# Kernel tuning notes

Measured on AMD Instinct MI355X. Metric: run time of the kernel, lower is better.

## Reference

```python
import math
import jax, jax.numpy as jnp
import numpy as np

OLEN = 512
RATIO = 0.5
DROP_P = 0.2


def _gat(x, src, dst, W, a_s, a_d, b):
    """PyG GATConv (heads=1, concat=True, add_self_loops=True, neg_slope=0.2)."""
    n = x.shape[0]
    loops = jnp.arange(n, dtype=src.dtype)
    s = jnp.concatenate([src, loops])  # [E+N] source nodes
    d = jnp.concatenate([dst, loops])  # [E+N] destination nodes
    h = x @ W                           # [N, H]
    alpha_s = h @ a_s                   # [N]
    alpha_d = h @ a_d                   # [N]
    e = jax.nn.leaky_relu(alpha_s[s] + alpha_d[d], 0.2)  # [E+N]
    # segment softmax over destination neighborhoods
    m = jax.ops.segment_max(e, d, num_segments=n)
    ee = jnp.exp(e - m[d])
    denom = jax.ops.segment_sum(ee, d, num_segments=n)
    alpha = ee / denom[d]
    out = jax.ops.segment_sum(alpha[:, None] * h[s], d, num_segments=n)
    return out + b


def _forward(x, src, dst, W1, a_src1, a_dst1, b1, W2, a_src2, a_dst2, b2,
             W3, a_src3, a_dst3, b3, W_rel, W_root, b_pool):
    N, E = x.shape[0], src.shape[0]
    key = jax.random.key(42)
    h = x
    for i, (W, a_s, a_d, b) in enumerate([(W1, a_src1, a_dst1, b1),
                                          (W2, a_src2, a_dst2, b2),
                                          (W3, a_src3, a_dst3, b3)]):
        h = jax.nn.relu(_gat(h, src, dst, W, a_s, a_d, b))
        keep = jax.random.bernoulli(jax.random.fold_in(key, i), 1.0 - DROP_P, h.shape)
        h = jnp.where(keep, h / (1.0 - DROP_P), 0.0)  # F.dropout(training=True)

    # SAGPooling(GraphConv score, ratio=0.5, tanh) repeated until n <= 512.
    # Node counts are static per iteration (k = ceil(0.5*n)); edge arrays keep
    # fixed size E with a validity mask (edges dropped when an endpoint is pooled away).
    cur_src, cur_dst = src, dst
    emask = jnp.ones((E,), dtype=h.dtype)
    n = N
    while True:
        agg = jax.ops.segment_sum(h[cur_src] * emask[:, None], cur_dst, num_segments=n)
        score = (agg @ W_rel + h @ W_root + b_pool)[:, 0]  # GraphConv(d->1), aggr='add'
        score = jnp.tanh(score)
        k = math.ceil(RATIO * n)
        top_vals, perm = jax.lax.top_k(score, k)
        h = h[perm] * top_vals[:, None]
        inv = jnp.full((n,), -1, dtype=cur_src.dtype).at[perm].set(
            jnp.arange(k, dtype=cur_src.dtype))
        ns, nd = inv[cur_src], inv[cur_dst]
        valid = (ns >= 0) & (nd >= 0)
        emask = emask * valid.astype(emask.dtype)
        cur_src = jnp.where(valid, ns, 0)
        cur_dst = jnp.where(valid, nd, 0)
        n = k
        if n <= OLEN:
            break

    out = jnp.zeros((OLEN, h.shape[1]), h.dtype).at[:n].set(h)
    return out


def setup_inputs() -> dict:
    key = jax.random.key(0)
    ks = jax.random.split(key, 20)
    N, E, IDIM, HDIM = 50000, 800000, 128, 200
    inp = {
        "x": jax.random.normal(ks[0], (N, IDIM), jnp.float32),
        "src": jax.random.randint(ks[1], (E,), 0, N, jnp.int32),
        "dst": jax.random.randint(ks[2], (E,), 0, N, jnp.int32),
    }
    def w(k, shape, fan_in):
        return jax.random.normal(k, shape, jnp.float32) / np.sqrt(fan_in).astype(np.float32)
    inp["W1"] = w(ks[3], (IDIM, HDIM), IDIM)
    inp["a_src1"] = w(ks[4], (HDIM,), HDIM)
    inp["a_dst1"] = w(ks[5], (HDIM,), HDIM)
    inp["b1"] = jnp.zeros((HDIM,), jnp.float32)
    inp["W2"] = w(ks[6], (HDIM, HDIM), HDIM)
    inp["a_src2"] = w(ks[7], (HDIM,), HDIM)
    inp["a_dst2"] = w(ks[8], (HDIM,), HDIM)
    inp["b2"] = jnp.zeros((HDIM,), jnp.float32)
    inp["W3"] = w(ks[9], (HDIM, HDIM), HDIM)
    inp["a_src3"] = w(ks[10], (HDIM,), HDIM)
    inp["a_dst3"] = w(ks[11], (HDIM,), HDIM)
    inp["b3"] = jnp.zeros((HDIM,), jnp.float32)
    inp["W_rel"] = w(ks[12], (HDIM, 1), HDIM)
    inp["W_root"] = w(ks[13], (HDIM, 1), HDIM)
    inp["b_pool"] = jnp.zeros((1,), jnp.float32)
    return inp


def reference(x, src, dst, W1, a_src1, a_dst1, b1, W2, a_src2, a_dst2, b2,
              W3, a_src3, a_dst3, b3, W_rel, W_root, b_pool):
    return _forward(x, src, dst, W1, a_src1, a_dst1, b1, W2, a_src2, a_dst2, b2,
                    W3, a_src3, a_dst3, b3, W_rel, W_root, b_pool)
```

## Files before the change

### kernel.cpp

```cpp
#include <hip/hip_runtime.h>
#include <cstdint>
#include <cstddef>


__host__ __device__ inline void tf_round(uint32_t &x0, uint32_t &x1, int r) {
  x0 += x1;
  x1 = (x1 << r) | (x1 >> (32 - r));
  x1 ^= x0;
}

__host__ __device__ inline void threefry2x32(uint32_t k0, uint32_t k1,
                                             uint32_t &x0, uint32_t &x1) {
  uint32_t ks2 = k0 ^ k1 ^ 0x1BD11BDAu;
  x0 += k0; x1 += k1;
  tf_round(x0, x1, 13); tf_round(x0, x1, 15); tf_round(x0, x1, 26); tf_round(x0, x1, 6);
  x0 += k1; x1 += ks2 + 1u;
  tf_round(x0, x1, 17); tf_round(x0, x1, 29); tf_round(x0, x1, 16); tf_round(x0, x1, 24);
  x0 += ks2; x1 += k0 + 2u;
  tf_round(x0, x1, 13); tf_round(x0, x1, 15); tf_round(x0, x1, 26); tf_round(x0, x1, 6);
  x0 += k0; x1 += k1 + 3u;
  tf_round(x0, x1, 17); tf_round(x0, x1, 29); tf_round(x0, x1, 16); tf_round(x0, x1, 24);
  x0 += k1; x1 += ks2 + 4u;
  tf_round(x0, x1, 13); tf_round(x0, x1, 15); tf_round(x0, x1, 26); tf_round(x0, x1, 6);
  x0 += ks2; x1 += k0 + 5u;
}

__global__ __launch_bounds__(256) void gemm200_k(
    const float* __restrict__ A, const float* __restrict__ B,
    float* __restrict__ C, int M, int K) {
  __shared__ float As[128 * 9];
  __shared__ __align__(16) float Bs[8][208];
  int tid = threadIdx.x;
  int m0 = blockIdx.x * 128;
  int r = tid >> 2;
  int colBase = (tid & 3) * 52;
  int nq = (colBase == 156) ? 11 : 13;
  float acc0[52], acc1[52];
#pragma unroll
  for (int q = 0; q < 52; q++) { acc0[q] = 0.f; acc1[q] = 0.f; }

  int arow = tid >> 1;
  int ac = (tid & 1) * 4;
  int gmA = m0 + arow;
  const float* Aptr = A + (size_t)gmA * K + ac;
  int bk0 = tid / 50, bc0 = (tid - bk0 * 50) * 4;
  int t2 = tid + 256;
  int bk1 = t2 / 50, bc1 = (t2 - bk1 * 50) * 4;
  bool hasB1 = (t2 < 400);

  float4 va = make_float4(0.f, 0.f, 0.f, 0.f);
  if (gmA < M) va = *(const float4*)(Aptr);
  float4 vb0 = *(const float4*)(B + (size_t)bk0 * 200 + bc0);
  float4 vb1 = make_float4(0.f, 0.f, 0.f, 0.f);
  if (hasB1) vb1 = *(const float4*)(B + (size_t)bk1 * 200 + bc1);

  for (int k0 = 0; k0 < K; k0 += 8) {
    As[arow * 9 + ac + 0] = va.x;
    As[arow * 9 + ac + 1] = va.y;
    As[arow * 9 + ac + 2] = va.z;
    As[arow * 9 + ac + 3] = va.w;
    *(float4*)(&Bs[bk0][bc0]) = vb0;
    if (hasB1) *(float4*)(&Bs[bk1][bc1]) = vb1;
    __syncthreads();
    int kn = k0 + 8;
    if (kn < K) {
      if (gmA < M) va = *(const float4*)(Aptr + kn);
      vb0 = *(const float4*)(B + (size_t)(kn + bk0) * 200 + bc0);
      if (hasB1) vb1 = *(const float4*)(B + (size_t)(kn + bk1) * 200 + bc1);
    }
#pragma unroll
    for (int kk = 0; kk < 8; kk++) {
      float a0 = As[r * 9 + kk];
      float a1 = As[(r + 64) * 9 + kk];
#pragma unroll
      for (int q = 0; q < 13; q++) {
        float4 b = *(const float4*)(&Bs[kk][colBase + 4 * q]);
        acc0[4 * q + 0] += a0 * b.x; acc0[4 * q + 1] += a0 * b.y;
        acc0[4 * q + 2] += a0 * b.z; acc0[4 * q + 3] += a0 * b.w;
        acc1[4 * q + 0] += a1 * b.x; acc1[4 * q + 1] += a1 * b.y;
        acc1[4 * q + 2] += a1 * b.z; acc1[4 * q + 3] += a1 * b.w;
      }
    }
    __syncthreads();
  }
  int gm0 = m0 + r, gm1 = m0 + r + 64;
#pragma unroll
  for (int q = 0; q < 13; q++) {
    if (q < nq) {
      int col = colBase + 4 * q;
      float4 v0 = make_float4(acc0[4 * q + 0], acc0[4 * q + 1],
                              acc0[4 * q + 2], acc0[4 * q + 3]);
      float4 v1 = make_float4(acc1[4 * q + 0], acc1[4 * q + 1],
                              acc1[4 * q + 2], acc1[4 * q + 3]);
      if (gm0 < M) *(float4*)(C + (size_t)gm0 * 200 + col) = v0;
      if (gm1 < M) *(float4*)(C + (size_t)gm1 * 200 + col) = v1;
    }
  }
}

__global__ __launch_bounds__(256) void dual_dot_k(
    const float* __restrict__ H, const float* __restrict__ v1,
    const float* __restrict__ v2, float* __restrict__ o1,
    float* __restrict__ o2, int n) {
  int wave = blockIdx.x * 4 + (threadIdx.x >> 6);
  int lane = threadIdx.x & 63;
  if (wave >= n) return;
  const float* row = H + (size_t)wave * 200;
  float s1 = 0.f, s2 = 0.f;
  for (int d = lane; d < 200; d += 64) {
    float h = row[d];
    s1 += h * v1[d];
    s2 += h * v2[d];
  }
  for (int off = 32; off; off >>= 1) {
    s1 += __shfl_down(s1, off);
    s2 += __shfl_down(s2, off);
  }
  if (lane == 0) { o1[wave] = s1; o2[wave] = s2; }
}

__global__ __launch_bounds__(256) void indeg_k(const int* __restrict__ dst,
                                               int* __restrict__ cnt, int E) {
  int e = blockIdx.x * 256 + threadIdx.x;
  if (e < E) atomicAdd(&cnt[dst[e]], 1);
}

__global__ __launch_bounds__(256) void scan_k(const int* __restrict__ cnt,
                                              int* __restrict__ rowptr, int N) {
  __shared__ int psum[256];
  int t = threadIdx.x;
  int CH = (N + 255) / 256;
  int beg = t * CH, end = min(beg + CH, N);
  if (beg > N) { beg = N; }
  int s = 0;
  for (int i = beg; i < end; i++) s += cnt[i];
  psum[t] = s;
  __syncthreads();
  if (t == 0) {
    int run = 0;
    for (int i = 0; i < 256; i++) { int v = psum[i]; psum[i] = run; run += v; }
  }
  __syncthreads();
  int run = psum[t];
  for (int i = beg; i < end; i++) { rowptr[i] = run; run += cnt[i]; }
  if (end == N && beg <= N) rowptr[N] = run;
}

__global__ __launch_bounds__(256) void cpyint_k(const int* __restrict__ a,
                                                int* __restrict__ b, int n) {
  int i = blockIdx.x * 256 + threadIdx.x;
  if (i < n) b[i] = a[i];
}

__global__ __launch_bounds__(256) void place_k(const int* __restrict__ dst,
                                               int* __restrict__ curs,
                                               int* __restrict__ csr, int E) {
  int e = blockIdx.x * 256 + threadIdx.x;
  if (e >= E) return;
  int pos = atomicAdd(&curs[dst[e]], 1);
  csr[pos] = e;
}

__global__ __launch_bounds__(256) void sortrow_k(const int* __restrict__ rowptr,
                                                 int* __restrict__ csr, int N) {
  int d = blockIdx.x * 256 + threadIdx.x;
  if (d >= N) return;
  int b = rowptr[d], e2 = rowptr[d + 1];
  for (int i = b + 1; i < e2; i++) {
    int v = csr[i];
    int j = i - 1;
    while (j >= b && csr[j] > v) { csr[j + 1] = csr[j]; j--; }
    csr[j + 1] = v;
  }
}

__device__ inline float dec_ord(unsigned enc) {
  unsigned b = (enc & 0x80000000u) ? (enc ^ 0x80000000u) : ~enc;
  return __uint_as_float(b);
}

__device__ inline unsigned enc_ord(float ev) {
  unsigned b = __float_as_uint(ev);
  return (b & 0x80000000u) ? ~b : (b | 0x80000000u);
}

__global__ __launch_bounds__(256) void eeden_k(
    const int* __restrict__ rowptr, const int* __restrict__ csr,
    const int* __restrict__ src, const float* __restrict__ as_,
    const float* __restrict__ ad_, int2* __restrict__ pk,
    float* __restrict__ eeS, float* __restrict__ den, int N) {
  int d = blockIdx.x * 256 + threadIdx.x;
  if (d >= N) return;
  float adv = ad_[d];
  int b = rowptr[d], e2 = rowptr[d + 1];
  unsigned mx = 0u;
  for (int i = b; i < e2; i++) {
    int sv = src[csr[i]];
    float v = as_[sv] + adv;
    float ev = (v >= 0.f) ? v : 0.2f * v;
    mx = max(mx, enc_ord(ev));
  }
  {
    float v = as_[d] + adv;
    float ev = (v >= 0.f) ? v : 0.2f * v;
    mx = max(mx, enc_ord(ev));
  }
  float m = dec_ord(mx);
  float s = 0.f;
  for (int i = b; i < e2; i++) {
    int sv = src[csr[i]];
    float v = as_[sv] + adv;
    float ev = (v >= 0.f) ? v : 0.2f * v;
    float ee = expf(ev - m);
    pk[i] = make_int2(sv, __float_as_int(ee));
    s = __fadd_rn(s, ee);
  }
  float vS = as_[d] + adv;
  float evS = (vS >= 0.f) ? vS : 0.2f * vS;
  float eS = expf(evS - m);
  eeS[d] = eS;
  s = __fadd_rn(s, eS);
  den[d] = s;
}

#define GLD(s) (*(const float4*)(Hl + (size_t)(s) * 200))
#define ACC(W_, H_)                                    \
  acc.x = __fadd_rn(acc.x, __fmul_rn((W_), (H_).x));   \
  acc.y = __fadd_rn(acc.y, __fmul_rn((W_), (H_).y));   \
  acc.z = __fadd_rn(acc.z, __fmul_rn((W_), (H_).z));   \
  acc.w = __fadd_rn(acc.w, __fmul_rn((W_), (H_).w));

__global__ __launch_bounds__(256) void gat_out_k(
    const int* __restrict__ rowptr, const int2* __restrict__ pk,
    const float* __restrict__ eeS, const float* __restrict__ den,
    const float* __restrict__ HW, const float* __restrict__ bias,
    float* __restrict__ OUT, uint32_t tk0, uint32_t tk1, int N) {
  int node = blockIdx.x * 4 + (threadIdx.x >> 6);
  int lane = threadIdx.x & 63;
  if (node >= N || lane >= 50) return;
  int b = rowptr[node];
  int deg = rowptr[node + 1] - b;
  int cnt = deg + 1;
  float dn = den[node];
  const float* __restrict__ Hl = HW + 4 * lane;

  auto fS = [&](int t, int &s, float &w) {
    if (t < deg) {
      int2 p = pk[b + t];
      s = p.x;
      w = __fdiv_rn(__int_as_float(p.y), dn);
    } else if (t == deg) {
      s = node;
      w = __fdiv_rn(eeS[node], dn);
    } else {
      s = node;
      w = 0.f;
    }
  };

  int sa, sb, sc, sd, se, sf, sn;
  float w0, w1, w2, w3, w4, w5, wn;
  fS(0, sa, w0); fS(1, sb, w1); fS(2, sc, w2); fS(3, sd, w3);
  float4 h0 = GLD(sa), h1 = GLD(sb), h2 = GLD(sc), h3 = GLD(sd);
  fS(4, se, w4);
  fS(5, sf, w5);

  float4 acc = make_float4(0.f, 0.f, 0.f, 0.f);
  for (int t = 0; t < cnt; t++) {
    float4 h4 = GLD(se);
    fS(t + 6, sn, wn);
    ACC(w0, h0);
    h0 = h1; h1 = h2; h2 = h3; h3 = h4;
    w0 = w1; w1 = w2; w2 = w3; w3 = w4; w4 = w5; w5 = wn;
    se = sf; sf = sn;
  }

  float4 bv4 = *(const float4*)(bias + 4 * lane);
  float vin[4] = {acc.x, acc.y, acc.z, acc.w};
  float bb4[4] = {bv4.x, bv4.y, bv4.z, bv4.w};
  float vout[4];
  int tbase = node * 200 + 4 * lane;
#pragma unroll
  for (int j = 0; j < 4; j++) {
    uint32_t x0 = 0u, x1 = (uint32_t)(tbase + j);
    threefry2x32(tk0, tk1, x0, x1);
    uint32_t bits = x0 ^ x1;
    float u = __uint_as_float((bits >> 9) | 0x3f800000u) - 1.0f;
    float v = vin[j] + bb4[j];
    v = fmaxf(v, 0.f);
    vout[j] = (u < 0.8f) ? (v / 0.8f) : 0.f;
  }
  *(float4*)(OUT + (size_t)node * 200 + 4 * lane) =
      make_float4(vout[0], vout[1], vout[2], vout[3]);
}

__global__ __launch_bounds__(256) void einit_k(
    const int* __restrict__ src, const int* __restrict__ dst,
    int* __restrict__ cs, int* __restrict__ cd, int* __restrict__ orig,
    int E, int N) {
  int e = blockIdx.x * 256 + threadIdx.x;
  if (e < E) { cs[e] = src[e]; cd[e] = dst[e]; }
  if (e < N) orig[e] = e;
}

__global__ __launch_bounds__(256) void pool_agg_k(
    const int* __restrict__ rowptr, const int* __restrict__ csr,
    const int* __restrict__ csrc, const int* __restrict__ orig,
    const float* __restrict__ H, const float* __restrict__ wrel,
    const float* __restrict__ wroot, const float* __restrict__ bp,
    float* __restrict__ score, int n) {
  __shared__ float sagg[4][200];
  int wv = threadIdx.x >> 6;
  int node = blockIdx.x * 4 + wv;
  int lane = threadIdx.x & 63;
  if (node >= n) return;
  int o = orig[node];
  int b = rowptr[o];
  int deg = rowptr[o + 1] - b;

  if (lane < 50) {
    const float* __restrict__ Hl = H + 4 * lane;
    auto fS = [&](int t, int &s, float &w) {
      if (t < deg) {
        int e = csr[b + t];
        int sv = csrc[e];
        s = (sv >= 0) ? sv : 0;
        w = (sv >= 0) ? 1.f : 0.f;
      } else {
        s = 0;
        w = 0.f;
      }
    };

    int sa, sb, sc, sd, se, sf, sn;
    float w0, w1, w2, w3, w4, w5, wn;
    fS(0, sa, w0); fS(1, sb, w1); fS(2, sc, w2); fS(3, sd, w3);
    float4 h0 = GLD(sa), h1 = GLD(sb), h2 = GLD(sc), h3 = GLD(sd);
    fS(4, se, w4);
    fS(5, sf, w5);

    float4 acc = make_float4(0.f, 0.f, 0.f, 0.f);
    for (int t = 0; t < deg; t++) {
      float4 h4 = GLD(se);
      fS(t + 6, sn, wn);
      ACC(w0, h0);
      h0 = h1; h1 = h2; h2 = h3; h3 = h4;
      w0 = w1; w1 = w2; w2 = w3; w3 = w4; w4 = w5; w5 = wn;
      se = sf; sf = sn;
    }
    sagg[wv][4 * lane + 0] = acc.x;
    sagg[wv][4 * lane + 1] = acc.y;
    sagg[wv][4 * lane + 2] = acc.z;
    sagg[wv][4 * lane + 3] = acc.w;
  }
  __threadfence_block();

  const float* arow = sagg[wv];
  const float* hrow = H + (size_t)node * 200;
  float s1 = 0.f, s2 = 0.f;
  for (int d = lane; d < 200; d += 64) {
    s1 += arow[d] * wrel[d];
    s2 += hrow[d] * wroot[d];
  }
  for (int off = 32; off; off >>= 1) {
    s1 += __shfl_down(s1, off);
    s2 += __shfl_down(s2, off);
  }
  if (lane == 0) score[node] = tanhf((s1 + s2) + bp[0]);
}
#undef GLD
#undef ACC


__global__ __launch_bounds__(256) void rhenc_k(const float* __restrict__ score,
                                               unsigned* __restrict__ keyA,
                                               int* __restrict__ payA,
                                               int* __restrict__ counts,
                                               int n, int NB) {
  __shared__ int hist[256];
  hist[threadIdx.x] = 0;
  __syncthreads();
  int i = blockIdx.x * 256 + threadIdx.x;
  if (i < n) {
    unsigned b = __float_as_uint(score[i]);
    if (b == 0x80000000u) b = 0u;
    unsigned key = ~enc_ord(__uint_as_float(b));
    keyA[i] = key;
    payA[i] = i;
    atomicAdd(&hist[key & 255u], 1);
  }
  __syncthreads();
  counts[threadIdx.x * NB + blockIdx.x] = hist[threadIdx.x];
}

__global__ __launch_bounds__(256) void rscan_k(int* __restrict__ counts,
                                               int* __restrict__ base, int NB) {
  __shared__ int tot[256];
  int t = threadIdx.x;
  int s = 0;
  for (int b = 0; b < NB; b++) s += counts[t * NB + b];
  tot[t] = s;
  __syncthreads();
  if (t == 0) {
    int run = 0;
    for (int i = 0; i < 256; i++) { int v = tot[i]; tot[i] = run; run += v; }
  }
  __syncthreads();
  int run = tot[t];
  for (int b = 0; b < NB; b++) {
    int c = counts[t * NB + b];
    base[t * NB + b] = run;
    run += c;
    counts[t * NB + b] = 0;
  }
}

__global__ __launch_bounds__(256) void rscatter_k(
    const unsigned* __restrict__ keyIn, const int* __restrict__ payIn,
    const int* __restrict__ base, unsigned* __restrict__ keyOut,
    int* __restrict__ payOut, int* __restrict__ countsNext,
    int n, int NB, int shift) {
  __shared__ int dig[256];
  int t = threadIdx.x;
  int i = blockIdx.x * 256 + t;
  unsigned k = 0u;
  int p = 0, d = -1;
  if (i < n) {
    k = keyIn[i];
    p = payIn[i];
    d = (int)((k >> shift) & 255u);
  }
  dig[t] = d;
  __syncthreads();
  if (i < n) {
    int local = 0;
    for (int j = 0; j < t; j++) local += (dig[j] == d) ? 1 : 0;
    int pos = base[d * NB + blockIdx.x] + local;
    keyOut[pos] = k;
    payOut[pos] = p;
    int nd = (int)((k >> (shift + 8)) & 255u);
    atomicAdd(&countsNext[nd * NB + (pos >> 8)], 1);
  }
}

__global__ __launch_bounds__(256) void rscatterF_k(
    const unsigned* __restrict__ keyIn, const int* __restrict__ payIn,
    const int* __restrict__ base, const int* __restrict__ oin,
    int* __restrict__ oout, int* __restrict__ perm, int* __restrict__ inv,
    int n, int NB, int k) {
  __shared__ int dig[256];
  int t = threadIdx.x;
  int i = blockIdx.x * 256 + t;
  int p = 0, d = -1;
  if (i < n) {
    p = payIn[i];
    d = (int)((keyIn[i] >> 24) & 255u);
  }
  dig[t] = d;
  __syncthreads();
  if (i < n) {
    int local = 0;
    for (int j = 0; j < t; j++) local += (dig[j] == d) ? 1 : 0;
    int pos = base[d * NB + blockIdx.x] + local;
    if (pos < k) { perm[pos] = p; inv[p] = pos; oout[pos] = oin[p]; }
    else inv[p] = -1;
  }
}

__global__ __launch_bounds__(256) void gather_k(
    const float* __restrict__ H, const int* __restrict__ perm,
    const float* __restrict__ score, float* __restrict__ Ho, int k) {
  int r = blockIdx.x;
  int d = threadIdx.x;
  int p = perm[r];
  float s = score[p];
  if (d < 200) Ho[(size_t)r * 200 + d] = __fmul_rn(H[(size_t)p * 200 + d], s);
}

__global__ __launch_bounds__(256) void remap_k(int* __restrict__ cs,
                                               int* __restrict__ cd,
                                               const int* __restrict__ inv, int E) {
  int e = blockIdx.x * 256 + threadIdx.x;
  if (e >= E) return;
  int a = cs[e];
  if (a < 0) return;
  int na = inv[a], nb = inv[cd[e]];
  bool valid = (na >= 0) && (nb >= 0);
  cs[e] = valid ? na : -1;
  cd[e] = valid ? nb : -1;
}

__global__ __launch_bounds__(256) void out_copy_k(const float* __restrict__ h,
                                                  float* __restrict__ out, int cnt) {
  int t = blockIdx.x * 256 + threadIdx.x;
  if (t < cnt) out[t] = h[t];
}

extern "C" void kernel_launch(void* const* d_in, const int* in_sizes, int n_in,
                              void* d_out, int out_size, void* d_ws, size_t ws_size,
                              hipStream_t stream) {
  const int ID = 128, HD = 200;
  const int N = in_sizes[0] / ID;
  const int E = in_sizes[1];

  const float* x = (const float*)d_in[0];
  const int* src = (const int*)d_in[1];
  const int* dst = (const int*)d_in[2];
  const float* W[3]   = {(const float*)d_in[3], (const float*)d_in[7], (const float*)d_in[11]};
  const float* asv[3] = {(const float*)d_in[4], (const float*)d_in[8], (const float*)d_in[12]};
  const float* adv[3] = {(const float*)d_in[5], (const float*)d_in[9], (const float*)d_in[13]};
  const float* bv[3]  = {(const float*)d_in[6], (const float*)d_in[10], (const float*)d_in[14]};
  const float* Wrel  = (const float*)d_in[15];
  const float* Wroot = (const float*)d_in[16];
  const float* bpool = (const float*)d_in[17];

  char* ws = (char*)d_ws;
  float*    bufA  = (float*)(ws + 0);
  float*    bufB  = (float*)(ws + 40000000);
  float*    as_   = (float*)(ws + 80000000);
  float*    ad_   = (float*)(ws + 80200000);
  float*    den   = (float*)(ws + 84000000);
  float*    score = (float*)(ws + 84200000);
  int*      rank_ = (int*)(ws + 84400000);
  int*      perm_ = (int*)(ws + 84600000);
  int*      inv_  = (int*)(ws + 84800000);
  int*      origA = (int*)(ws + 85000000);
  int*      origB = (int*)(ws + 85200000);
  int*      rowptr= (int*)(ws + 85400000);
  int*      curs  = (int*)(ws + 85650000);
  int*      csr   = (int*)(ws + 85850000);
  int*      csrc  = (int*)(ws + 89050000);
  int*      cdst  = (int*)(ws + 92250000);

  int2* pk = (int2*)(ws + 89050000);
  float* eeS = (float*)(ws + 80400000);

  char* rx = ws + 80400000;
  unsigned* keyA   = (unsigned*)(rx + 0 * 262144);
  unsigned* keyB   = (unsigned*)(rx + 1 * 262144);
  int*      payA   = (int*)(rx + 2 * 262144);
  int*      payB   = (int*)(rx + 3 * 262144);
  int*      rcounts= (int*)(rx + 4 * 262144);
  int*      rbase  = (int*)(rx + 5 * 262144);

  uint32_t fk0[3], fk1[3];
  for (int i = 0; i < 3; i++) {
    uint32_t a = 0u, b = (uint32_t)i;
    threefry2x32(0u, 42u, a, b);
    fk0[i] = a; fk1[i] = b;
  }

  const int B256 = 256;
  hipMemsetAsync(rank_, 0, (size_t)N * 4, stream);
  indeg_k<<<(E + 255) / 256, B256, 0, stream>>>(dst, rank_, E);
  scan_k<<<1, B256, 0, stream>>>(rank_, rowptr, N);
  cpyint_k<<<(N + 255) / 256, B256, 0, stream>>>(rowptr, curs, N);
  place_k<<<(E + 255) / 256, B256, 0, stream>>>(dst, curs, csr, E);
  sortrow_k<<<(N + 255) / 256, B256, 0, stream>>>(rowptr, csr, N);

  for (int i = 0; i < 3; i++) {
    const float* in = (i == 0) ? x : bufB;
    int K = (i == 0) ? ID : HD;
    gemm200_k<<<(N + 127) / 128, B256, 0, stream>>>(in, W[i], bufA, N, K);
    dual_dot_k<<<(N + 3) / 4, B256, 0, stream>>>(bufA, asv[i], adv[i], as_, ad_, N);
    eeden_k<<<(N + 255) / 256, B256, 0, stream>>>(rowptr, csr, src, as_, ad_,
                                                  pk, eeS, den, N);
    gat_out_k<<<(N + 3) / 4, B256, 0, stream>>>(rowptr, pk, eeS, den, bufA,
                                                bv[i], bufB, fk0[i], fk1[i], N);
  }

  einit_k<<<(E + 255) / 256, B256, 0, stream>>>(src, dst, csrc, cdst, origA, E, N);
  float* hcur = bufB;
  float* hnext = bufA;
  int* ocur = origA;
  int* onext = origB;
  int n = N;
  while (true) {
    int k = (n + 1) / 2;
    int NB = (n + 255) / 256;
    pool_agg_k<<<(n + 3) / 4, B256, 0, stream>>>(rowptr, csr, csrc, ocur, hcur,
                                                 Wrel, Wroot, bpool, score, n);
    rhenc_k<<<NB, B256, 0, stream>>>(score, keyA, payA, rcounts, n, NB);
    rscan_k<<<1, B256, 0, stream>>>(rcounts, rbase, NB);
    rscatter_k<<<NB, B256, 0, stream>>>(keyA, payA, rbase, keyB, payB, rcounts, n, NB, 0);
    rscan_k<<<1, B256, 0, stream>>>(rcounts, rbase, NB);
    rscatter_k<<<NB, B256, 0, stream>>>(keyB, payB, rbase, keyA, payA, rcounts, n, NB, 8);
    rscan_k<<<1, B256, 0, stream>>>(rcounts, rbase, NB);
    rscatter_k<<<NB, B256, 0, stream>>>(keyA, payA, rbase, keyB, payB, rcounts, n, NB, 16);
    rscan_k<<<1, B256, 0, stream>>>(rcounts, rbase, NB);
    rscatterF_k<<<NB, B256, 0, stream>>>(keyB, payB, rbase, ocur, onext, perm_, inv_,
                                         n, NB, k);
    gather_k<<<k, B256, 0, stream>>>(hcur, perm_, score, hnext, k);
    remap_k<<<(E + 255) / 256, B256, 0, stream>>>(csrc, cdst, inv_, E);
    { float* t = hcur; hcur = hnext; hnext = t; }
    { int* t = ocur; ocur = onext; onext = t; }
    n = k;
    if (n <= 512) break;
  }

  hipMemsetAsync(d_out, 0, (size_t)out_size * 4, stream);
  out_copy_k<<<(n * HD + 255) / 256, B256, 0, stream>>>(hcur, (float*)d_out, n * HD);
}
```

Baseline: 2.699 ms.

## Halve GEMM row tile and fuse small kernels to cut launches

```diff
diff --git a/kernel.cpp b/kernel.cpp
--- a/kernel.cpp
+++ b/kernel.cpp
@@ -28,19 +28,20 @@
 __global__ __launch_bounds__(256) void gemm200_k(
     const float* __restrict__ A, const float* __restrict__ B,
     float* __restrict__ C, int M, int K) {
-  __shared__ float As[128 * 9];
+  __shared__ float As[64 * 9];
   __shared__ __align__(16) float Bs[8][208];
   int tid = threadIdx.x;
-  int m0 = blockIdx.x * 128;
+  int m0 = blockIdx.x * 64;
   int r = tid >> 2;
   int colBase = (tid & 3) * 52;
   int nq = (colBase == 156) ? 11 : 13;
-  float acc0[52], acc1[52];
+  float acc[52];
 #pragma unroll
-  for (int q = 0; q < 52; q++) { acc0[q] = 0.f; acc1[q] = 0.f; }
+  for (int q = 0; q < 52; q++) acc[q] = 0.f;
 
   int arow = tid >> 1;
   int ac = (tid & 1) * 4;
+  bool hasA = (tid < 128);
   int gmA = m0 + arow;
   const float* Aptr = A + (size_t)gmA * K + ac;
   int bk0 = tid / 50, bc0 = (tid - bk0 * 50) * 4;
@@ -49,51 +50,47 @@
   bool hasB1 = (t2 < 400);
 
   float4 va = make_float4(0.f, 0.f, 0.f, 0.f);
-  if (gmA < M) va = *(const float4*)(Aptr);
+  if (hasA && gmA < M) va = *(const float4*)(Aptr);
   float4 vb0 = *(const float4*)(B + (size_t)bk0 * 200 + bc0);
   float4 vb1 = make_float4(0.f, 0.f, 0.f, 0.f);
   if (hasB1) vb1 = *(const float4*)(B + (size_t)bk1 * 200 + bc1);
 
   for (int k0 = 0; k0 < K; k0 += 8) {
-    As[arow * 9 + ac + 0] = va.x;
-    As[arow * 9 + ac + 1] = va.y;
-    As[arow * 9 + ac + 2] = va.z;
-    As[arow * 9 + ac + 3] = va.w;
+    if (hasA) {
+      As[arow * 9 + ac + 0] = va.x;
+      As[arow * 9 + ac + 1] = va.y;
+      As[arow * 9 + ac + 2] = va.z;
+      As[arow * 9 + ac + 3] = va.w;
+    }
     *(float4*)(&Bs[bk0][bc0]) = vb0;
     if (hasB1) *(float4*)(&Bs[bk1][bc1]) = vb1;
     __syncthreads();
     int kn = k0 + 8;
     if (kn < K) {
-      if (gmA < M) va = *(const float4*)(Aptr + kn);
+      if (hasA && gmA < M) va = *(const float4*)(Aptr + kn);
       vb0 = *(const float4*)(B + (size_t)(kn + bk0) * 200 + bc0);
       if (hasB1) vb1 = *(const float4*)(B + (size_t)(kn + bk1) * 200 + bc1);
     }
 #pragma unroll
     for (int kk = 0; kk < 8; kk++) {
       float a0 = As[r * 9 + kk];
-      float a1 = As[(r + 64) * 9 + kk];
 #pragma unroll
       for (int q = 0; q < 13; q++) {
         float4 b = *(const float4*)(&Bs[kk][colBase + 4 * q]);
-        acc0[4 * q + 0] += a0 * b.x; acc0[4 * q + 1] += a0 * b.y;
-        acc0[4 * q + 2] += a0 * b.z; acc0[4 * q + 3] += a0 * b.w;
-        acc1[4 * q + 0] += a1 * b.x; acc1[4 * q + 1] += a1 * b.y;
-        acc1[4 * q + 2] += a1 * b.z; acc1[4 * q + 3] += a1 * b.w;
+        acc[4 * q + 0] += a0 * b.x; acc[4 * q + 1] += a0 * b.y;
+        acc[4 * q + 2] += a0 * b.z; acc[4 * q + 3] += a0 * b.w;
       }
     }
     __syncthreads();
   }
-  int gm0 = m0 + r, gm1 = m0 + r + 64;
+  int gm = m0 + r;
 #pragma unroll
   for (int q = 0; q < 13; q++) {
     if (q < nq) {
       int col = colBase + 4 * q;
-      float4 v0 = make_float4(acc0[4 * q + 0], acc0[4 * q + 1],
-                              acc0[4 * q + 2], acc0[4 * q + 3]);
-      float4 v1 = make_float4(acc1[4 * q + 0], acc1[4 * q + 1],
-                              acc1[4 * q + 2], acc1[4 * q + 3]);
-      if (gm0 < M) *(float4*)(C + (size_t)gm0 * 200 + col) = v0;
-      if (gm1 < M) *(float4*)(C + (size_t)gm1 * 200 + col) = v1;
+      float4 v0 = make_float4(acc[4 * q + 0], acc[4 * q + 1],
+                              acc[4 * q + 2], acc[4 * q + 3]);
+      if (gm < M) *(float4*)(C + (size_t)gm * 200 + col) = v0;
     }
   }
 }
@@ -126,7 +123,8 @@
 }
 
 __global__ __launch_bounds__(256) void scan_k(const int* __restrict__ cnt,
-                                              int* __restrict__ rowptr, int N) {
+                                              int* __restrict__ rowptr,
+                                              int* __restrict__ curs, int N) {
   __shared__ int psum[256];
   int t = threadIdx.x;
   int CH = (N + 255) / 256;
@@ -142,14 +140,12 @@
   }
   __syncthreads();
   int run = psum[t];
-  for (int i = beg; i < end; i++) { rowptr[i] = run; run += cnt[i]; }
+  for (int i = beg; i < end; i++) {
+    rowptr[i] = run;
+    curs[i] = run;
+    run += cnt[i];
+  }
   if (end == N && beg <= N) rowptr[N] = run;
-}
-
-__global__ __launch_bounds__(256) void cpyint_k(const int* __restrict__ a,
-                                                int* __restrict__ b, int n) {
-  int i = blockIdx.x * 256 + threadIdx.x;
-  if (i < n) b[i] = a[i];
 }
 
 __global__ __launch_bounds__(256) void place_k(const int* __restrict__ dst,
@@ -317,7 +313,6 @@
   int o = orig[node];
   int b = rowptr[o];
   int deg = rowptr[o + 1] - b;
-
   if (lane < 50) {
     const float* __restrict__ Hl = H + 4 * lane;
     auto fS = [&](int t, int &s, float &w) {
@@ -331,14 +326,12 @@
         w = 0.f;
       }
     };
-
     int sa, sb, sc, sd, se, sf, sn;
     float w0, w1, w2, w3, w4, w5, wn;
     fS(0, sa, w0); fS(1, sb, w1); fS(2, sc, w2); fS(3, sd, w3);
     float4 h0 = GLD(sa), h1 = GLD(sb), h2 = GLD(sc), h3 = GLD(sd);
     fS(4, se, w4);
     fS(5, sf, w5);
-
     float4 acc = make_float4(0.f, 0.f, 0.f, 0.f);
     for (int t = 0; t < deg; t++) {
       float4 h4 = GLD(se);
@@ -354,7 +347,6 @@
     sagg[wv][4 * lane + 3] = acc.w;
   }
   __threadfence_block();
-
   const float* arow = sagg[wv];
   const float* hrow = H + (size_t)node * 200;
   float s1 = 0.f, s2 = 0.f;
@@ -370,7 +362,6 @@
 }
 #undef GLD
 #undef ACC
-
 
 __global__ __launch_bounds__(256) void rhenc_k(const float* __restrict__ score,
                                                unsigned* __restrict__ keyA,
@@ -438,8 +429,7 @@
     int pos = base[d * NB + blockIdx.x] + local;
     keyOut[pos] = k;
     payOut[pos] = p;
-    int nd = (int)((k >> (shift + 8)) & 255u);
-    atomicAdd(&countsNext[nd * NB + (pos >> 8)], 1);
+    atomicAdd(&countsNext[((k >> (shift + 8)) & 255u) * NB + (pos >> 8)], 1);
   }
 }
 
@@ -467,33 +457,37 @@
   }
 }
 
-__global__ __launch_bounds__(256) void gather_k(
+__global__ __launch_bounds__(256) void gr_k(
     const float* __restrict__ H, const int* __restrict__ perm,
-    const float* __restrict__ score, float* __restrict__ Ho, int k) {
-  int r = blockIdx.x;
-  int d = threadIdx.x;
-  int p = perm[r];
-  float s = score[p];
-  if (d < 200) Ho[(size_t)r * 200 + d] = __fmul_rn(H[(size_t)p * 200 + d], s);
-}
-
-__global__ __launch_bounds__(256) void remap_k(int* __restrict__ cs,
-                                               int* __restrict__ cd,
-                                               const int* __restrict__ inv, int E) {
-  int e = blockIdx.x * 256 + threadIdx.x;
-  if (e >= E) return;
-  int a = cs[e];
-  if (a < 0) return;
-  int na = inv[a], nb = inv[cd[e]];
-  bool valid = (na >= 0) && (nb >= 0);
-  cs[e] = valid ? na : -1;
-  cd[e] = valid ? nb : -1;
+    const float* __restrict__ score, float* __restrict__ Ho,
+    int* __restrict__ cs, int* __restrict__ cd, const int* __restrict__ inv,
+    int k, int E) {
+  int bidx = blockIdx.x;
+  if (bidx < k) {
+    int d = threadIdx.x;
+    int p = perm[bidx];
+    float s = score[p];
+    if (d < 200)
+      Ho[(size_t)bidx * 200 + d] = __fmul_rn(H[(size_t)p * 200 + d], s);
+  } else {
+    int e = (bidx - k) * 256 + threadIdx.x;
+    if (e < E) {
+      int a = cs[e];
+      if (a >= 0) {
+        int na = inv[a], nb = inv[cd[e]];
+        bool valid = (na >= 0) && (nb >= 0);
+        cs[e] = valid ? na : -1;
+        cd[e] = valid ? nb : -1;
+      }
+    }
+  }
 }
 
 __global__ __launch_bounds__(256) void out_copy_k(const float* __restrict__ h,
-                                                  float* __restrict__ out, int cnt) {
+                                                  float* __restrict__ out,
+                                                  int cnt, int total) {
   int t = blockIdx.x * 256 + threadIdx.x;
-  if (t < cnt) out[t] = h[t];
+  if (t < total) out[t] = (t < cnt) ? h[t] : 0.f;
 }
 
 extern "C" void kernel_launch(void* const* d_in, const int* in_sizes, int n_in,
@@ -553,15 +547,14 @@
   const int B256 = 256;
   hipMemsetAsync(rank_, 0, (size_t)N * 4, stream);
   indeg_k<<<(E + 255) / 256, B256, 0, stream>>>(dst, rank_, E);
-  scan_k<<<1, B256, 0, stream>>>(rank_, rowptr, N);
-  cpyint_k<<<(N + 255) / 256, B256, 0, stream>>>(rowptr, curs, N);
+  scan_k<<<1, B256, 0, stream>>>(rank_, rowptr, curs, N);
   place_k<<<(E + 255) / 256, B256, 0, stream>>>(dst, curs, csr, E);
   sortrow_k<<<(N + 255) / 256, B256, 0, stream>>>(rowptr, csr, N);
 
   for (int i = 0; i < 3; i++) {
     const float* in = (i == 0) ? x : bufB;
     int K = (i == 0) ? ID : HD;
-    gemm200_k<<<(N + 127) / 128, B256, 0, stream>>>(in, W[i], bufA, N, K);
+    gemm200_k<<<(N + 63) / 64, B256, 0, stream>>>(in, W[i], bufA, N, K);
     dual_dot_k<<<(N + 3) / 4, B256, 0, stream>>>(bufA, asv[i], adv[i], as_, ad_, N);
     eeden_k<<<(N + 255) / 256, B256, 0, stream>>>(rowptr, csr, src, as_, ad_,
                                                   pk, eeS, den, N);
@@ -590,14 +583,14 @@
     rscan_k<<<1, B256, 0, stream>>>(rcounts, rbase, NB);
     rscatterF_k<<<NB, B256, 0, stream>>>(keyB, payB, rbase, ocur, onext, perm_, inv_,
                                          n, NB, k);
-    gather_k<<<k, B256, 0, stream>>>(hcur, perm_, score, hnext, k);
-    remap_k<<<(E + 255) / 256, B256, 0, stream>>>(csrc, cdst, inv_, E);
+    gr_k<<<k + (E + 255) / 256, B256, 0, stream>>>(hcur, perm_, score, hnext,
+                                                   csrc, cdst, inv_, k, E);
     { float* t = hcur; hcur = hnext; hnext = t; }
     { int* t = ocur; ocur = onext; onext = t; }
     n = k;
     if (n <= 512) break;
   }
 
-  hipMemsetAsync(d_out, 0, (size_t)out_size * 4, stream);
-  out_copy_k<<<(n * HD + 255) / 256, B256, 0, stream>>>(hcur, (float*)d_out, n * HD);
-}
+  out_copy_k<<<(out_size + 255) / 256, B256, 0, stream>>>(hcur, (float*)d_out,
+                                                          n * HD, out_size);
+}
```

Measured after the change: 2.763 ms. +2.4%, slower.
